# Kernel tuning notes

Measured on AMD Instinct MI355X. Metric: run time of the kernel, lower is better.

Reference implementation:

```python
import jax, jax.numpy as jnp
import numpy as np
from jax import lax

B = 32768
L = 200          # window_size
K = 5            # conv kernel
CIN = 6
FLAT = L - K + 1  # 196, conv1d valid output length (out channels = 1)


def setup_inputs() -> dict:
    key = jax.random.key(0)
    ks = jax.random.split(key, 9)
    s = lambda *sh: 1.0 / np.sqrt(sh[-1])
    x = jax.random.normal(ks[0], (B, CIN, L), dtype=jnp.float32)
    conv_w = jax.random.normal(ks[1], (1, CIN, K), dtype=jnp.float32) * (1.0 / np.sqrt(CIN * K))
    conv_b = jax.random.normal(ks[2], (1,), dtype=jnp.float32) * 0.1
    w1 = jax.random.normal(ks[3], (FLAT, 50), dtype=jnp.float32) * (1.0 / np.sqrt(FLAT))
    b1 = jax.random.normal(ks[4], (50,), dtype=jnp.float32) * 0.1
    w2 = jax.random.normal(ks[5], (50, 30), dtype=jnp.float32) * (1.0 / np.sqrt(50))
    b2 = jax.random.normal(ks[6], (30,), dtype=jnp.float32) * 0.1
    w3 = jax.random.normal(ks[7], (30, 15), dtype=jnp.float32) * (1.0 / np.sqrt(30))
    b3 = jax.random.normal(ks[8], (15,), dtype=jnp.float32) * 0.1
    return {"x": x, "conv_w": conv_w, "conv_b": conv_b, "w1": w1, "b1": b1,
            "w2": w2, "b2": b2, "w3": w3, "b3": b3}


def reference(x, conv_w, conv_b, w1, b1, w2, b2, w3, b3):
    # conv1d (valid): [B,6,200] -> [B,1,196]
    y = lax.conv_general_dilated(x, conv_w, window_strides=(1,), padding='VALID',
                                 dimension_numbers=('NCH', 'OIH', 'NCH'))
    y = y + conv_b[None, :, None]
    h = y.reshape(x.shape[0], -1)                       # [B,196]
    h = jax.nn.relu(h @ w1 + b1)                        # [B,50]
    h = jax.nn.relu(h @ w2 + b2)                        # [B,30]
    out = h @ w3 + b3                                   # [B,15]
    # Procrustes orthogonalization of the 3x3 block
    R = out[:, :9].reshape(-1, 3, 3)
    U, _, VT = jnp.linalg.svd(R)                        # batched 3x3 SVD
    det = jnp.linalg.det(jnp.matmul(U, VT))             # [B]
    scale = jnp.stack([jnp.ones_like(det), jnp.ones_like(det), det], axis=1)  # diag(1,1,det)
    R_norm = jnp.matmul(U, VT * scale[:, :, None])      # U @ S @ VT
    return jnp.concatenate([R_norm.reshape(-1, 9), out[:, 9:]], axis=1)
```

## Files before the change

kernel.cpp:

```cpp
#include <hip/hip_runtime.h>
#include <math.h>

#define BATCH 32768
#define LW    200
#define CIN   6
#define KSZ   5
#define FLAT  196
#define NH1   50
#define NH2   30
#define NOUT  15
#define XROW  (CIN * LW)


__device__ __forceinline__ float fget(const float4 (&a)[8], int i) {
    const float4 v = a[i >> 2];
    const int m = i & 3;
    return m == 0 ? v.x : (m == 1 ? v.y : (m == 2 ? v.z : v.w));
}

__global__ void __launch_bounds__(64)
conv_fc1_k7(const float* __restrict__ x,
            const float* __restrict__ cw, const float* __restrict__ cb,
            const float* __restrict__ w1, float* __restrict__ part)
{
    const int lane = threadIdx.x;
    const int bid  = blockIdx.x;
    const int r  = bid & 7;
    const int q  = bid >> 3;
    const int gq = q / 7;
    const int s  = q - gq * 7;
    const int g  = r * 64 + gq;
    const int kstart = 28 * s;

    float w[CIN][KSZ];
#pragma unroll
    for (int c = 0; c < CIN; ++c)
#pragma unroll
        for (int k = 0; k < KSZ; ++k)
            w[c][k] = __int_as_float(
                __builtin_amdgcn_readfirstlane(__float_as_int(cw[c * KSZ + k])));
    const float bias = __int_as_float(
        __builtin_amdgcn_readfirstlane(__float_as_int(cb[0])));

    const float* xb = x + (size_t)(g * 64 + lane) * XROW + kstart;

    float acc[28];
#pragma unroll
    for (int i = 0; i < 28; ++i) acc[i] = bias;

    float4 A[8], B[8];
#pragma unroll
    for (int u = 0; u < 8; ++u)
        A[u] = *(const float4*)(xb + 4 * u);

#pragma unroll
    for (int ch = 0; ch < CIN; ch += 2) {
#pragma unroll
        for (int u = 0; u < 8; ++u)
            B[u] = *(const float4*)(xb + (ch + 1) * LW + 4 * u);
#pragma unroll
        for (int i = 0; i < 28; ++i) {
            float a = acc[i];
            a = fmaf(fget(A, i + 0), w[ch][0], a);
            a = fmaf(fget(A, i + 1), w[ch][1], a);
            a = fmaf(fget(A, i + 2), w[ch][2], a);
            a = fmaf(fget(A, i + 3), w[ch][3], a);
            a = fmaf(fget(A, i + 4), w[ch][4], a);
            acc[i] = a;
        }
        if (ch + 2 < CIN) {
#pragma unroll
            for (int u = 0; u < 8; ++u)
                A[u] = *(const float4*)(xb + (ch + 2) * LW + 4 * u);
        }
#pragma unroll
        for (int i = 0; i < 28; ++i) {
            float a = acc[i];
            a = fmaf(fget(B, i + 0), w[ch + 1][0], a);
            a = fmaf(fget(B, i + 1), w[ch + 1][1], a);
            a = fmaf(fget(B, i + 2), w[ch + 1][2], a);
            a = fmaf(fget(B, i + 3), w[ch + 1][3], a);
            a = fmaf(fget(B, i + 4), w[ch + 1][4], a);
            acc[i] = a;
        }
    }

    float* pb = part + (size_t)(s * NH1) * BATCH + (size_t)g * 64 + lane;
#pragma unroll
    for (int half = 0; half < 2; ++half) {
        const int j0 = half * 25;
        float h1p[25];
#pragma unroll
        for (int j = 0; j < 25; ++j) h1p[j] = 0.f;
#pragma unroll
        for (int ii = 0; ii < 28; ii += 2) {
            const float* wr0 = w1 + (size_t)(kstart + ii) * NH1 + j0;
            const float* wr1 = wr0 + NH1;
            float c0 = acc[ii], c1 = acc[ii + 1];
#pragma unroll
            for (int j = 0; j < 25; ++j)
                h1p[j] = fmaf(c1, wr1[j], fmaf(c0, wr0[j], h1p[j]));
        }
#pragma unroll
        for (int j = 0; j < 25; ++j)
            pb[(size_t)(j0 + j) * BATCH] = h1p[j];
    }
}

template<int NS, int TB, int NLD, int TW, int NSPLIT>
__device__ __forceinline__ void conv_fc1_body(
    const float* __restrict__ x,
    const float* __restrict__ cw, const float* __restrict__ cb,
    const float* __restrict__ w1, float* __restrict__ part,
    float* __restrict__ tile)
{
    const int lane = threadIdx.x;
    const int bid  = blockIdx.x;
    const int r = bid & 7;
    const int q = bid >> 3;
    const int g = r * 64 + q / NSPLIT;
    const int s = q - (q / NSPLIT) * NSPLIT;
    const int kstart = NS * s;
    const int tbase  = TB * s;
    const int off    = kstart - tbase;

    float w[CIN][KSZ];
#pragma unroll
    for (int c = 0; c < CIN; ++c)
#pragma unroll
        for (int k = 0; k < KSZ; ++k)
            w[c][k] = __int_as_float(
                __builtin_amdgcn_readfirstlane(__float_as_int(cw[c * KSZ + k])));
    const float bias = __int_as_float(
        __builtin_amdgcn_readfirstlane(__float_as_int(cb[0])));

    int goff[NLD], loff[NLD];
#pragma unroll
    for (int u = 0; u < NLD; ++u) {
        int g4  = lane + 64 * u;
        int row = g4 / NLD;
        int c4  = g4 - row * NLD;
        goff[u] = row * XROW + 4 * c4;
        loff[u] = row * TW + 4 * c4;
    }
    const float* xw = x + (size_t)g * 64 * XROW + tbase;

    float acc[NS];
#pragma unroll
    for (int i = 0; i < NS; ++i) acc[i] = bias;

    float4 buf[NLD];
#pragma unroll
    for (int u = 0; u < NLD; ++u) buf[u] = *(const float4*)(xw + goff[u]);

#pragma unroll
    for (int ch = 0; ch < CIN; ++ch) {
#pragma unroll
        for (int u = 0; u < NLD; ++u) {
            float* dst = tile + loff[u];
            dst[0] = buf[u].x; dst[1] = buf[u].y; dst[2] = buf[u].z; dst[3] = buf[u].w;
        }
        if (ch + 1 < CIN) {
#pragma unroll
            for (int u = 0; u < NLD; ++u)
                buf[u] = *(const float4*)(xw + (ch + 1) * LW + goff[u]);
        }
        const float* row = tile + lane * TW + off;
        float x0 = row[0], x1 = row[1], x2 = row[2], x3 = row[3];
#pragma unroll
        for (int i = 0; i < NS; ++i) {
            float x4v = row[i + 4];
            float a = acc[i];
            a = fmaf(x0, w[ch][0], a);
            a = fmaf(x1, w[ch][1], a);
            a = fmaf(x2, w[ch][2], a);
            a = fmaf(x3, w[ch][3], a);
            a = fmaf(x4v, w[ch][4], a);
            acc[i] = a;
            x0 = x1; x1 = x2; x2 = x3; x3 = x4v;
        }
    }

    float* pb = part + (size_t)(s * NH1) * BATCH + (size_t)g * 64 + lane;
#pragma unroll
    for (int half = 0; half < 2; ++half) {
        const int j0 = half * 25;
        float h1p[25];
#pragma unroll
        for (int j = 0; j < 25; ++j) h1p[j] = 0.f;
#pragma unroll
        for (int ii = 0; ii < NS; ++ii) {
            const float* wrow = w1 + (size_t)(kstart + ii) * NH1 + j0;
            float c = acc[ii];
#pragma unroll
            for (int j = 0; j < 25; ++j) h1p[j] = fmaf(c, wrow[j], h1p[j]);
        }
#pragma unroll
        for (int j = 0; j < 25; ++j)
            pb[(size_t)(j0 + j) * BATCH] = h1p[j];
    }
}

__global__ void __launch_bounds__(64)
conv_fc1_k4(const float* __restrict__ x,
            const float* __restrict__ cw, const float* __restrict__ cb,
            const float* __restrict__ w1, float* __restrict__ part)
{
    __shared__ float tile[64 * 57];
    conv_fc1_body<49, 48, 14, 57, 4>(x, cw, cb, w1, part, tile);
}

__global__ void __launch_bounds__(64)
conv_fc1_k2(const float* __restrict__ x,
            const float* __restrict__ cw, const float* __restrict__ cb,
            const float* __restrict__ w1, float* __restrict__ part)
{
    __shared__ float tile[64 * 105];
    conv_fc1_body<98, 96, 26, 105, 2>(x, cw, cb, w1, part, tile);
}

template<int NSPLIT>
__global__ void __launch_bounds__(64)
tail_kernel(
    const float* __restrict__ part,
    const float* __restrict__ b1,
    const float* __restrict__ w2, const float* __restrict__ b2,
    const float* __restrict__ w3, const float* __restrict__ b3,
    float* __restrict__ out)
{
    const int bid = blockIdx.x;
    const int g   = (bid & 7) * 64 + (bid >> 3);
    const int b   = g * 64 + threadIdx.x;
    const float* pb = part + b;

    float h2[NH2];
#pragma unroll
    for (int j = 0; j < NH2; ++j) h2[j] = b2[j];

#pragma unroll
    for (int k = 0; k < NH1; ++k) {
        float a = b1[k];
#pragma unroll
        for (int s = 0; s < NSPLIT; ++s)
            a += pb[(size_t)(s * NH1 + k) * BATCH];
        float hk = fmaxf(a, 0.f);
        const float* row = w2 + k * NH2;
#pragma unroll
        for (int j = 0; j < NH2; ++j) h2[j] = fmaf(hk, row[j], h2[j]);
    }
#pragma unroll
    for (int j = 0; j < NH2; ++j) h2[j] = fmaxf(h2[j], 0.f);

    float o[NOUT];
#pragma unroll
    for (int j = 0; j < NOUT; ++j) o[j] = b3[j];
#pragma unroll
    for (int k = 0; k < NH2; ++k) {
        float hk = h2[k];
        const float* row = w3 + k * NOUT;
#pragma unroll
        for (int j = 0; j < NOUT; ++j) o[j] = fmaf(hk, row[j], o[j]);
    }

    float r00 = o[0], r01 = o[1], r02 = o[2];
    float r10 = o[3], r11 = o[4], r12 = o[5];
    float r20 = o[6], r21 = o[7], r22 = o[8];

    float A[4][4], V[4][4];
    A[0][0] = r00 + r11 + r22;
    A[1][1] = r00 - r11 - r22;
    A[2][2] = r11 - r00 - r22;
    A[3][3] = r22 - r00 - r11;
    A[0][1] = A[1][0] = r21 - r12;
    A[0][2] = A[2][0] = r02 - r20;
    A[0][3] = A[3][0] = r10 - r01;
    A[1][2] = A[2][1] = r01 + r10;
    A[1][3] = A[3][1] = r02 + r20;
    A[2][3] = A[3][2] = r12 + r21;
#pragma unroll
    for (int i = 0; i < 4; ++i)
#pragma unroll
        for (int j = 0; j < 4; ++j) V[i][j] = (i == j) ? 1.f : 0.f;

    const int pr[6][2] = {{0,1},{0,2},{0,3},{1,2},{1,3},{2,3}};
    for (int sweep = 0; sweep < 7; ++sweep) {
#pragma unroll
        for (int pi = 0; pi < 6; ++pi) {
            const int p = pr[pi][0], qq = pr[pi][1];
            float apq = A[p][qq];
            if (fabsf(apq) > 1e-20f) {
                float theta = (A[qq][qq] - A[p][p]) / (2.f * apq);
                float t = copysignf(1.f, theta) / (fabsf(theta) + sqrtf(1.f + theta * theta));
                float c = rsqrtf(1.f + t * t);
                float sn = t * c;
#pragma unroll
                for (int k = 0; k < 4; ++k) {
                    float akp = A[k][p], akq = A[k][qq];
                    A[k][p] = c * akp - sn * akq;
                    A[k][qq] = sn * akp + c * akq;
                }
#pragma unroll
                for (int k = 0; k < 4; ++k) {
                    float apk = A[p][k], aqk = A[qq][k];
                    A[p][k] = c * apk - sn * aqk;
                    A[qq][k] = sn * apk + c * aqk;
                }
#pragma unroll
                for (int k = 0; k < 4; ++k) {
                    float vkp = V[k][p], vkq = V[k][qq];
                    V[k][p] = c * vkp - sn * vkq;
                    V[k][qq] = sn * vkp + c * vkq;
                }
            }
        }
    }

    int best = 0;
    float bl = A[0][0];
#pragma unroll
    for (int i = 1; i < 4; ++i)
        if (A[i][i] > bl) { bl = A[i][i]; best = i; }

    float vsel[4];
#pragma unroll
    for (int k = 0; k < 4; ++k) {
        float v = V[k][0];
        v = (best == 1) ? V[k][1] : v;
        v = (best == 2) ? V[k][2] : v;
        v = (best == 3) ? V[k][3] : v;
        vsel[k] = v;
    }
    float vw = vsel[0], vx = vsel[1], vy = vsel[2], vz = vsel[3];
    float inv = rsqrtf(vw * vw + vx * vx + vy * vy + vz * vz);
    vw *= inv; vx *= inv; vy *= inv; vz *= inv;

    float xx = vx * vx, yy = vy * vy, zz = vz * vz;
    float xy = vx * vy, xz = vx * vz, yz = vy * vz;
    float wx = vw * vx, wy = vw * vy, wz = vw * vz;

    float* ob = out + (long)b * NOUT;
    ob[0]  = 1.f - 2.f * (yy + zz);
    ob[1]  = 2.f * (xy - wz);
    ob[2]  = 2.f * (xz + wy);
    ob[3]  = 2.f * (xy + wz);
    ob[4]  = 1.f - 2.f * (xx + zz);
    ob[5]  = 2.f * (yz - wx);
    ob[6]  = 2.f * (xz - wy);
    ob[7]  = 2.f * (yz + wx);
    ob[8]  = 1.f - 2.f * (xx + yy);
    ob[9]  = o[9];
    ob[10] = o[10];
    ob[11] = o[11];
    ob[12] = o[12];
    ob[13] = o[13];
    ob[14] = o[14];
}

extern "C" void kernel_launch(void* const* d_in, const int* in_sizes, int n_in,
                              void* d_out, int out_size, void* d_ws, size_t ws_size,
                              hipStream_t stream) {
    const float* x  = (const float*)d_in[0];
    const float* cw = (const float*)d_in[1];
    const float* cb = (const float*)d_in[2];
    const float* w1 = (const float*)d_in[3];
    const float* b1 = (const float*)d_in[4];
    const float* w2 = (const float*)d_in[5];
    const float* b2 = (const float*)d_in[6];
    const float* w3 = (const float*)d_in[7];
    const float* b3 = (const float*)d_in[8];
    float* outp = (float*)d_out;
    float* part = (float*)d_ws;

    const size_t need7 = (size_t)7 * NH1 * BATCH * sizeof(float);
    const size_t need4 = (size_t)4 * NH1 * BATCH * sizeof(float);

    if (ws_size >= need7) {
        conv_fc1_k7<<<7 * (BATCH / 64), 64, 0, stream>>>(x, cw, cb, w1, part);
        tail_kernel<7><<<BATCH / 64, 64, 0, stream>>>(part, b1, w2, b2, w3, b3, outp);
    } else if (ws_size >= need4) {
        conv_fc1_k4<<<4 * (BATCH / 64), 64, 0, stream>>>(x, cw, cb, w1, part);
        tail_kernel<4><<<BATCH / 64, 64, 0, stream>>>(part, b1, w2, b2, w3, b3, outp);
    } else {
        conv_fc1_k2<<<2 * (BATCH / 64), 64, 0, stream>>>(x, cw, cb, w1, part);
        tail_kernel<2><<<BATCH / 64, 64, 0, stream>>>(part, b1, w2, b2, w3, b3, outp);
    }
}
```

Before: 329.0 us.

## Split tail reduction across four lanes per sample and reorder conv FMA chains

The tail kernel now assigns four lanes to each batch element. The lanes split the reads of the fc1 partial sums by split index, combine them with xor shuffles, and share the 15 output stores. This gives four times as many blocks, which adds parallelism and memory-level concurrency for the latency-bound partial-sum reads. The cost is that the small MLP and eigen-solver work is duplicated four ways. The conv loop in the k7 kernel is also manually unrolled with an interleaved accumulator order, meant to improve instruction-level parallelism.

```diff
diff --git a/kernel.cpp b/kernel.cpp
--- a/kernel.cpp
+++ b/kernel.cpp
@@ -17,6 +17,24 @@
     const int m = i & 3;
     return m == 0 ? v.x : (m == 1 ? v.y : (m == 2 ? v.z : v.w));
 }
+
+#define CONVSTEP(R, CH)                                        \
+    _Pragma("unroll")                                          \
+    for (int ii = 0; ii < 28; ++ii) {                          \
+        const int i = (4 * ii) % 28 + (4 * ii) / 28;           \
+        float aa = acc[i];                                     \
+        aa = fmaf(fget(R, i + 0), w[CH][0], aa);               \
+        aa = fmaf(fget(R, i + 1), w[CH][1], aa);               \
+        aa = fmaf(fget(R, i + 2), w[CH][2], aa);               \
+        aa = fmaf(fget(R, i + 3), w[CH][3], aa);               \
+        aa = fmaf(fget(R, i + 4), w[CH][4], aa);               \
+        acc[i] = aa;                                           \
+    }
+
+#define LOADCH(R, CH)                                          \
+    _Pragma("unroll")                                          \
+    for (int u = 0; u < 8; ++u)                                \
+        R[u] = *(const float4*)(xb + (CH) * LW + 4 * u);
 
 __global__ void __launch_bounds__(64)
 conv_fc1_k7(const float* __restrict__ x,
@@ -49,41 +67,19 @@
     for (int i = 0; i < 28; ++i) acc[i] = bias;
 
     float4 A[8], B[8];
-#pragma unroll
-    for (int u = 0; u < 8; ++u)
-        A[u] = *(const float4*)(xb + 4 * u);
-
-#pragma unroll
-    for (int ch = 0; ch < CIN; ch += 2) {
-#pragma unroll
-        for (int u = 0; u < 8; ++u)
-            B[u] = *(const float4*)(xb + (ch + 1) * LW + 4 * u);
-#pragma unroll
-        for (int i = 0; i < 28; ++i) {
-            float a = acc[i];
-            a = fmaf(fget(A, i + 0), w[ch][0], a);
-            a = fmaf(fget(A, i + 1), w[ch][1], a);
-            a = fmaf(fget(A, i + 2), w[ch][2], a);
-            a = fmaf(fget(A, i + 3), w[ch][3], a);
-            a = fmaf(fget(A, i + 4), w[ch][4], a);
-            acc[i] = a;
-        }
-        if (ch + 2 < CIN) {
-#pragma unroll
-            for (int u = 0; u < 8; ++u)
-                A[u] = *(const float4*)(xb + (ch + 2) * LW + 4 * u);
-        }
-#pragma unroll
-        for (int i = 0; i < 28; ++i) {
-            float a = acc[i];
-            a = fmaf(fget(B, i + 0), w[ch + 1][0], a);
-            a = fmaf(fget(B, i + 1), w[ch + 1][1], a);
-            a = fmaf(fget(B, i + 2), w[ch + 1][2], a);
-            a = fmaf(fget(B, i + 3), w[ch + 1][3], a);
-            a = fmaf(fget(B, i + 4), w[ch + 1][4], a);
-            acc[i] = a;
-        }
-    }
+    LOADCH(A, 0)
+    LOADCH(B, 1)
+
+    CONVSTEP(A, 0)
+    LOADCH(A, 2)
+    CONVSTEP(B, 1)
+    LOADCH(B, 3)
+    CONVSTEP(A, 2)
+    LOADCH(A, 4)
+    CONVSTEP(B, 3)
+    LOADCH(B, 5)
+    CONVSTEP(A, 4)
+    CONVSTEP(B, 5)
 
     float* pb = part + (size_t)(s * NH1) * BATCH + (size_t)g * 64 + lane;
 #pragma unroll
@@ -228,22 +224,41 @@
     const float* __restrict__ w3, const float* __restrict__ b3,
     float* __restrict__ out)
 {
-    const int bid = blockIdx.x;
-    const int g   = (bid & 7) * 64 + (bid >> 3);
-    const int b   = g * 64 + threadIdx.x;
-    const float* pb = part + b;
+    const int t    = threadIdx.x;
+    const int bid  = blockIdx.x;
+    const int gidx = (bid & 7) * 256 + (bid >> 3);
+    const int bsub = t >> 2;
+    const int role = t & 3;
+    const int b    = gidx * 16 + bsub;
+
+    float a[NH1];
+#pragma unroll
+    for (int k = 0; k < NH1; ++k) a[k] = 0.f;
+#pragma unroll
+    for (int ss = 0; ss < (NSPLIT + 3) / 4; ++ss) {
+        const int s = role + 4 * ss;
+        if (s < NSPLIT) {
+            const float* ps = part + (size_t)s * NH1 * BATCH + b;
+#pragma unroll
+            for (int k = 0; k < NH1; ++k)
+                a[k] += ps[(size_t)k * BATCH];
+        }
+    }
+
+#pragma unroll
+    for (int k = 0; k < NH1; ++k) {
+        float v = a[k];
+        v += __shfl_xor(v, 1, 64);
+        v += __shfl_xor(v, 2, 64);
+        a[k] = v;
+    }
 
     float h2[NH2];
 #pragma unroll
     for (int j = 0; j < NH2; ++j) h2[j] = b2[j];
-
 #pragma unroll
     for (int k = 0; k < NH1; ++k) {
-        float a = b1[k];
-#pragma unroll
-        for (int s = 0; s < NSPLIT; ++s)
-            a += pb[(size_t)(s * NH1 + k) * BATCH];
-        float hk = fmaxf(a, 0.f);
+        float hk = fmaxf(a[k] + b1[k], 0.f);
         const float* row = w2 + k * NH2;
 #pragma unroll
         for (int j = 0; j < NH2; ++j) h2[j] = fmaf(hk, row[j], h2[j]);
@@ -290,9 +305,9 @@
             float apq = A[p][qq];
             if (fabsf(apq) > 1e-20f) {
                 float theta = (A[qq][qq] - A[p][p]) / (2.f * apq);
-                float t = copysignf(1.f, theta) / (fabsf(theta) + sqrtf(1.f + theta * theta));
-                float c = rsqrtf(1.f + t * t);
-                float sn = t * c;
+                float tt = copysignf(1.f, theta) / (fabsf(theta) + sqrtf(1.f + theta * theta));
+                float c = rsqrtf(1.f + tt * tt);
+                float sn = tt * c;
 #pragma unroll
                 for (int k = 0; k < 4; ++k) {
                     float akp = A[k][p], akq = A[k][qq];
@@ -338,22 +353,27 @@
     float xy = vx * vy, xz = vx * vz, yz = vy * vz;
     float wx = vw * vx, wy = vw * vy, wz = vw * vz;
 
-    float* ob = out + (long)b * NOUT;
-    ob[0]  = 1.f - 2.f * (yy + zz);
-    ob[1]  = 2.f * (xy - wz);
-    ob[2]  = 2.f * (xz + wy);
-    ob[3]  = 2.f * (xy + wz);
-    ob[4]  = 1.f - 2.f * (xx + zz);
-    ob[5]  = 2.f * (yz - wx);
-    ob[6]  = 2.f * (xz - wy);
-    ob[7]  = 2.f * (yz + wx);
-    ob[8]  = 1.f - 2.f * (xx + yy);
-    ob[9]  = o[9];
-    ob[10] = o[10];
-    ob[11] = o[11];
-    ob[12] = o[12];
-    ob[13] = o[13];
-    ob[14] = o[14];
+    float res[NOUT];
+    res[0]  = 1.f - 2.f * (yy + zz);
+    res[1]  = 2.f * (xy - wz);
+    res[2]  = 2.f * (xz + wy);
+    res[3]  = 2.f * (xy + wz);
+    res[4]  = 1.f - 2.f * (xx + zz);
+    res[5]  = 2.f * (yz - wx);
+    res[6]  = 2.f * (xz - wy);
+    res[7]  = 2.f * (yz + wx);
+    res[8]  = 1.f - 2.f * (xx + yy);
+    res[9]  = o[9];
+    res[10] = o[10];
+    res[11] = o[11];
+    res[12] = o[12];
+    res[13] = o[13];
+    res[14] = o[14];
+
+    float* ob = out + (size_t)b * NOUT;
+#pragma unroll
+    for (int j = 0; j < NOUT; ++j)
+        if ((j & 3) == role) ob[j] = res[j];
 }
 
 extern "C" void kernel_launch(void* const* d_in, const int* in_sizes, int n_in,
@@ -376,12 +396,12 @@
 
     if (ws_size >= need7) {
         conv_fc1_k7<<<7 * (BATCH / 64), 64, 0, stream>>>(x, cw, cb, w1, part);
-        tail_kernel<7><<<BATCH / 64, 64, 0, stream>>>(part, b1, w2, b2, w3, b3, outp);
+        tail_kernel<7><<<BATCH / 16, 64, 0, stream>>>(part, b1, w2, b2, w3, b3, outp);
     } else if (ws_size >= need4) {
         conv_fc1_k4<<<4 * (BATCH / 64), 64, 0, stream>>>(x, cw, cb, w1, part);
-        tail_kernel<4><<<BATCH / 64, 64, 0, stream>>>(part, b1, w2, b2, w3, b3, outp);
+        tail_kernel<4><<<BATCH / 16, 64, 0, stream>>>(part, b1, w2, b2, w3, b3, outp);
     } else {
         conv_fc1_k2<<<2 * (BATCH / 64), 64, 0, stream>>>(x, cw, cb, w1, part);
-        tail_kernel<2><<<BATCH / 64, 64, 0, stream>>>(part, b1, w2, b2, w3, b3, outp);
-    }
-}
+        tail_kernel<2><<<BATCH / 16, 64, 0, stream>>>(part, b1, w2, b2, w3, b3, outp);
+    }
+}
```

Result: slower. 338.1 us (+2.8%).
